# Optimization experiments

Measured on AMD Instinct MI355X. Metric: run time of the kernel, lower is better.

The kernel has to match this reference:

```python
import jax, jax.numpy as jnp
import numpy as np
import math

B, S, DIM = 2, 2048, 4096
N_HEADS, N_KV_HEADS = 32, 8
HEAD_DIM = DIM // N_HEADS  # 128
N_REP = N_HEADS // N_KV_HEADS  # 4
ROPE_THETA = 10000.0


def setup_inputs() -> dict:
    key = jax.random.key(0)
    ks = jax.random.split(key, 6)
    x = jax.random.normal(ks[0], (B, S, DIM), dtype=jnp.float32)
    wq = jax.random.normal(ks[1], (DIM, DIM), dtype=jnp.float32) * 0.02
    wk = jax.random.normal(ks[2], (N_KV_HEADS * HEAD_DIM, DIM), dtype=jnp.float32) * 0.02
    wv = jax.random.normal(ks[3], (N_KV_HEADS * HEAD_DIM, DIM), dtype=jnp.float32) * 0.02
    wo = jax.random.normal(ks[4], (DIM, DIM), dtype=jnp.float32) * 0.02
    # rotary freqs_cis (seqlen, head_dim//2), represented as cos/sin
    inv_freq = 1.0 / (ROPE_THETA ** (jnp.arange(0, HEAD_DIM, 2, dtype=jnp.float32) / HEAD_DIM))
    angles = jnp.arange(S, dtype=jnp.float32)[:, None] * inv_freq[None, :]  # [S, HEAD_DIM//2]
    freqs_cos = jnp.cos(angles)
    freqs_sin = jnp.sin(angles)
    # additive causal mask [S, S]: 0 on/below diagonal, -inf above
    mask = jnp.where(jnp.tril(jnp.ones((S, S), dtype=bool)), 0.0, -jnp.inf).astype(jnp.float32)
    return {"x": x, "wq": wq, "wk": wk, "wv": wv, "wo": wo,
            "freqs_cos": freqs_cos, "freqs_sin": freqs_sin, "mask": mask}


def _apply_rotary(t, freqs_cos, freqs_sin):
    # t: [B, S, H, HEAD_DIM]; interpret pairs (even, odd) as complex
    t2 = t.reshape(*t.shape[:-1], HEAD_DIM // 2, 2)
    tr, ti = t2[..., 0], t2[..., 1]
    c = freqs_cos[None, :, None, :]  # [1, S, 1, HD/2]
    s = freqs_sin[None, :, None, :]
    out_r = tr * c - ti * s
    out_i = tr * s + ti * c
    return jnp.stack([out_r, out_i], axis=-1).reshape(t.shape)


def reference(x, wq, wk, wv, wo, freqs_cos, freqs_sin, mask):
    bsz, seqlen, _ = x.shape
    xq = (x @ wq.T).reshape(bsz, seqlen, N_HEADS, HEAD_DIM)
    xk = (x @ wk.T).reshape(bsz, seqlen, N_KV_HEADS, HEAD_DIM)
    xv = (x @ wv.T).reshape(bsz, seqlen, N_KV_HEADS, HEAD_DIM)
    xq = _apply_rotary(xq, freqs_cos, freqs_sin)
    xk = _apply_rotary(xk, freqs_cos, freqs_sin)
    # repeat_kv (GQA): [B,S,KV,HD] -> [B,S,KV*N_REP,HD] via repeat_interleave on head axis
    keys = jnp.repeat(xk, N_REP, axis=2)
    values = jnp.repeat(xv, N_REP, axis=2)
    # scores: [B, H, S, S]
    scores = jnp.einsum('bqhd,bkhd->bhqk', xq, keys) / math.sqrt(HEAD_DIM)
    scores = scores + mask[None, None, :, :]
    probs = jax.nn.softmax(scores.astype(jnp.float32), axis=-1).astype(xq.dtype)
    out = jnp.einsum('bhqk,bkhd->bqhd', probs, values).reshape(bsz, seqlen, DIM)
    return out @ wo.T
```

## Files before the change

### kernel.cpp

```cpp
#include <hip/hip_runtime.h>

typedef __bf16 bf16;
typedef __bf16 bf16x4 __attribute__((ext_vector_type(4)));
typedef __bf16 bf16x8 __attribute__((ext_vector_type(8)));
typedef float f32x4 __attribute__((ext_vector_type(4)));

#define BB 2
#define SS 2048
#define DIM 4096
#define KVDIM 1024
#define NH 32
#define NKV 8
#define HD 128
#define NEGINF (-1e30f)

__device__ __forceinline__ void async16(void* lds, const void* gmem) {
    __builtin_amdgcn_global_load_lds(
        (const __attribute__((address_space(1))) void*)gmem,
        (__attribute__((address_space(3))) void*)lds, 16, 0, 0);
}

__device__ __forceinline__ f32x4 mfma16(bf16x8 a, bf16x8 b, f32x4 c) {
    return __builtin_amdgcn_mfma_f32_16x16x32_bf16(a, b, c, 0, 0, 0);
}

struct DetectArgs { const void* p[7]; int n[7]; };

__global__ void detect_dtypes(DetectArgs a, int* flags) {
    __shared__ int bad;
    const int ti = blockIdx.x;
    if (threadIdx.x == 0) bad = 0;
    __syncthreads();
    const bf16* s = (const bf16*)a.p[ti];
    int n = a.n[ti];
    int take = n < 8192 ? n : 8192;
    int lbad = 0;
    for (int i = threadIdx.x; i < take; i += 256) {
        float f = (float)s[i];
        if (!(f > -1e4f && f < 1e4f)) lbad = 1;
    }
    if (lbad) atomicOr(&bad, 1);
    __syncthreads();
    if (threadIdx.x == 0) flags[ti] = bad;
}

__global__ void convert_to_bf16(const void* __restrict__ src, bf16* __restrict__ dst,
                                int n8, const int* __restrict__ flagp) {
    int i = blockIdx.x * 256 + threadIdx.x;
    if (i >= n8) return;
    if (*flagp) {
        const float* s = (const float*)src + (size_t)i * 8;
        bf16x8 v;
#pragma unroll
        for (int j = 0; j < 8; ++j) v[j] = (bf16)s[j];
        *(bf16x8*)(dst + (size_t)i * 8) = v;
    } else {
        *(bf16x8*)(dst + (size_t)i * 8) = *((const bf16x8*)src + i);
    }
}

#define SBAR()  asm volatile("s_barrier" ::: "memory")
#define LGKM0() asm volatile("s_waitcnt lgkmcnt(0)" ::: "memory")
#define VM4()   asm volatile("s_waitcnt vmcnt(4)" ::: "memory")
#define VM0()   asm volatile("s_waitcnt vmcnt(0)" ::: "memory")

__device__ __forceinline__ void gemm256_core(const bf16* __restrict__ A,
                                             const bf16* __restrict__ B,
                                             int K, int m0, int n0,
                                             f32x4 (&acc)[8][4]) {
    __shared__ bf16 sm[2][4][8192];
    const int t = threadIdx.x;
    const int lane = t & 63;
    const int w = t >> 6;
    const int l15 = lane & 15, quad = lane >> 4;
    const int wm = w >> 2;
    const int wn = w & 3;
    const int axr = l15 & 7;
    const int c0 = (quad ^ axr) * 8;
    const int c1 = ((4 + quad) ^ axr) * 8;
    const int srl = t >> 3;
    const int sch = ((t & 7) ^ (srl & 7)) * 8;
    const size_t Ks = (size_t)K;

    bf16x8 aReg[4][2], bReg[4][2];

#define RD_A(c_, mh) { \
    const bf16* ab = &sm[c_][wm][0] + ((mh) * 64 + l15) * 64; \
    _Pragma("unroll") for (int i = 0; i < 4; ++i) { \
        aReg[i][0] = *(const bf16x8*)(ab + i * 1024 + c0); \
        aReg[i][1] = *(const bf16x8*)(ab + i * 1024 + c1); } }

#define RD_B(c_, nh) { \
    const bf16* bb = &sm[c_][2 + (wn >> 1)][0] + ((wn & 1) * 64 + (nh) * 32 + l15) * 64; \
    _Pragma("unroll") for (int jj = 0; jj < 2; ++jj) { \
        bReg[(nh) * 2 + jj][0] = *(const bf16x8*)(bb + jj * 1024 + c0); \
        bReg[(nh) * 2 + jj][1] = *(const bf16x8*)(bb + jj * 1024 + c1); } }

#define STG(c_, reg_, Mat, rowbase, kt) { \
    bf16* d_ = &sm[c_][reg_][0] + (size_t)t * 8; \
    const bf16* s_ = (Mat) + ((size_t)((rowbase) + srl)) * Ks + (size_t)(kt) * 64 + sch; \
    async16(d_, s_); \
    async16(d_ + 4096, s_ + 64 * Ks); }

#define MM(mh, nh) { \
    _Pragma("unroll") for (int i = 0; i < 4; ++i) \
    _Pragma("unroll") for (int jj = 0; jj < 2; ++jj) { \
        acc[(mh) * 4 + i][(nh) * 2 + jj] = \
            mfma16(aReg[i][0], bReg[(nh) * 2 + jj][0], acc[(mh) * 4 + i][(nh) * 2 + jj]); \
        acc[(mh) * 4 + i][(nh) * 2 + jj] = \
            mfma16(aReg[i][1], bReg[(nh) * 2 + jj][1], acc[(mh) * 4 + i][(nh) * 2 + jj]); } }

    STG(0, 0, A, m0, 0);
    STG(0, 2, B, n0, 0);
    STG(0, 1, A, m0 + 128, 0);
    STG(0, 3, B, n0 + 128, 0);
    STG(1, 2, B, n0, 1);
    STG(1, 0, A, m0, 1);
    VM4(); SBAR();

    const int NT = K >> 6;
    for (int T = 0; T < NT; ++T) {
        const int c = T & 1, nc = c ^ 1;
        const int kt1 = (T + 1 < NT) ? T + 1 : 0;
        const int kt2 = (T + 2 < NT) ? T + 2 : 0;
        RD_A(c, 0); RD_B(c, 0);
        STG(nc, 1, A, m0 + 128, kt1);
        SBAR();
        __builtin_amdgcn_s_setprio(1); MM(0, 0); __builtin_amdgcn_s_setprio(0);
        LGKM0(); SBAR();
        RD_B(c, 1);
        STG(nc, 3, B, n0 + 128, kt1);
        SBAR();
        __builtin_amdgcn_s_setprio(1); MM(0, 1); __builtin_amdgcn_s_setprio(0);
        LGKM0(); SBAR();
        RD_A(c, 1);
        STG(c, 2, B, n0, kt2);
        SBAR();
        __builtin_amdgcn_s_setprio(1); MM(1, 0); __builtin_amdgcn_s_setprio(0);
        LGKM0(); SBAR();
        STG(c, 0, A, m0, kt2);
        SBAR();
        __builtin_amdgcn_s_setprio(1); MM(1, 1); __builtin_amdgcn_s_setprio(0);
        LGKM0(); VM4(); SBAR();
    }
#undef RD_A
#undef RD_B
#undef STG
#undef MM
}

__global__ __launch_bounds__(512, 2)
void gemm_nt(const bf16* __restrict__ A, const bf16* __restrict__ B,
             bf16* __restrict__ C, int M, int N, int K) {
    const int t = threadIdx.x, lane = t & 63, w = t >> 6;
    const int l15 = lane & 15, quad = lane >> 4;
    const int wm = w >> 2, wn = w & 3;
    const int m0 = blockIdx.y * 256, n0 = blockIdx.x * 256;
    f32x4 acc[8][4] = {};
    gemm256_core(A, B, K, m0, n0, acc);
#pragma unroll
    for (int i = 0; i < 8; ++i)
#pragma unroll
        for (int j = 0; j < 4; ++j) {
            int col = n0 + wn * 64 + j * 16 + l15;
#pragma unroll
            for (int r = 0; r < 4; ++r)
                C[(size_t)(m0 + wm * 128 + i * 16 + quad * 4 + r) * N + col] = (bf16)acc[i][j][r];
        }
}

__global__ __launch_bounds__(512, 2)
void gemm_nt_kv(const bf16* __restrict__ A, const bf16* __restrict__ Bkv,
                bf16* __restrict__ Kc, bf16* __restrict__ Vc, int M, int K) {
    const int t = threadIdx.x, lane = t & 63, w = t >> 6;
    const int l15 = lane & 15, quad = lane >> 4;
    const int wm = w >> 2, wn = w & 3;
    const int m0 = blockIdx.y * 256, n0 = blockIdx.x * 256;
    f32x4 acc[8][4] = {};
    gemm256_core(A, Bkv, K, m0, n0, acc);
    bf16* C = (n0 < KVDIM) ? Kc : Vc;
    const int cb = (n0 < KVDIM) ? n0 : n0 - KVDIM;
#pragma unroll
    for (int i = 0; i < 8; ++i)
#pragma unroll
        for (int j = 0; j < 4; ++j) {
            int col = cb + wn * 64 + j * 16 + l15;
#pragma unroll
            for (int r = 0; r < 4; ++r)
                C[(size_t)(m0 + wm * 128 + i * 16 + quad * 4 + r) * KVDIM + col] = (bf16)acc[i][j][r];
        }
}

__global__ __launch_bounds__(512, 2)
void gemm_nt_out(const bf16* __restrict__ A, const bf16* __restrict__ B,
                 void* __restrict__ C, int M, int N, int K,
                 const int* __restrict__ flagp) {
    const int t = threadIdx.x, lane = t & 63, w = t >> 6;
    const int l15 = lane & 15, quad = lane >> 4;
    const int wm = w >> 2, wn = w & 3;
    const int m0 = blockIdx.y * 256, n0 = blockIdx.x * 256;
    const int f32out = *flagp;
    f32x4 acc[8][4] = {};
    gemm256_core(A, B, K, m0, n0, acc);
#pragma unroll
    for (int i = 0; i < 8; ++i)
#pragma unroll
        for (int j = 0; j < 4; ++j) {
            int col = n0 + wn * 64 + j * 16 + l15;
#pragma unroll
            for (int r = 0; r < 4; ++r) {
                int row = m0 + wm * 128 + i * 16 + quad * 4 + r;
                if (f32out) ((float*)C)[(size_t)row * N + col] = acc[i][j][r];
                else        ((bf16*)C)[(size_t)row * N + col] = (bf16)acc[i][j][r];
            }
        }
}

__device__ __forceinline__ void rope8(bf16* p, const bf16* fc, const bf16* fs,
                                      int s, int i0, float sc) {
    bf16x8 v = *(bf16x8*)p;
    bf16x8 o;
#pragma unroll
    for (int j = 0; j < 4; ++j) {
        float tr = (float)v[2 * j], ti = (float)v[2 * j + 1];
        float cc = (float)fc[s * 64 + i0 + j];
        float sn = (float)fs[s * 64 + i0 + j];
        o[2 * j]     = (bf16)((tr * cc - ti * sn) * sc);
        o[2 * j + 1] = (bf16)((tr * sn + ti * cc) * sc);
    }
    *(bf16x8*)p = o;
}

__global__ void rope_kernel(bf16* __restrict__ Q, bf16* __restrict__ Kr,
                            const bf16* __restrict__ fc, const bf16* __restrict__ fs) {
    const float qscale = 0.08838834764831845f * 1.4426950408889634f;
    int u = blockIdx.x * 256 + threadIdx.x;
    const int QU = (DIM * (BB * SS)) / 8;
    if (u < QU) {
        int row = u >> 9;
        int c = (u & 511) * 8;
        rope8(Q + (size_t)row * DIM + c, fc, fs, row & (SS - 1), (c >> 1) & 63, qscale);
    } else {
        u -= QU;
        int row = u >> 7;
        int c = (u & 127) * 8;
        rope8(Kr + (size_t)row * KVDIM + c, fc, fs, row & (SS - 1), (c >> 1) & 63, 1.0f);
    }
}

__global__ void transpose_v(const bf16* __restrict__ V, bf16* __restrict__ Vt) {
    __shared__ bf16 tile[64][74];
    const int st = blockIdx.x, ct = blockIdx.y, b = blockIdx.z;
    const int s0 = st * 64;
    const int kvh = ct >> 1, d0 = (ct & 1) * 64;
    const int t = threadIdx.x;
#pragma unroll
    for (int i = 0; i < 2; ++i) {
        int o = i * 256 + t;
        int r = o >> 3, c8 = (o & 7) * 8;
        bf16x8 v = *(const bf16x8*)(V + (size_t)(b * SS + s0 + r) * KVDIM + kvh * HD + d0 + c8);
#pragma unroll
        for (int j = 0; j < 8; ++j) tile[r][c8 + j] = v[j];
    }
    __syncthreads();
#pragma unroll
    for (int i = 0; i < 2; ++i) {
        int o = i * 256 + t;
        int sseg = (o & 7) * 8, dl = o >> 3;
        bf16x8 v;
#pragma unroll
        for (int j = 0; j < 8; ++j) v[j] = tile[sseg + j][dl];
        *(bf16x8*)(Vt + ((size_t)((b * NKV + kvh) * HD) + d0 + dl) * SS + s0 + sseg) = v;
    }
}

__global__ __launch_bounds__(256, 2)
void flash_attn(const bf16* __restrict__ Q, const bf16* __restrict__ Kr,
                const bf16* __restrict__ Vt, bf16* __restrict__ AO) {
    __shared__ char smem[32768];
    bf16* Ks  = (bf16*)smem;
    bf16* Vts = (bf16*)(smem + 16384);
    char* Ps  = smem;
    const int t = threadIdx.x, w = t >> 6, lane = t & 63;
    const int l15 = lane & 15, quad = lane >> 4;
    const int bh = blockIdx.x;
    const int b = bh >> 5, h = bh & 31, kvh = h >> 2;
    const int q0 = ((int)gridDim.y - 1 - (int)blockIdx.y) * 128;

    bf16x8 qf[2][4];
#pragma unroll
    for (int mi = 0; mi < 2; ++mi) {
        int qrow = b * SS + q0 + w * 32 + mi * 16 + l15;
#pragma unroll
        for (int ks = 0; ks < 4; ++ks)
            qf[mi][ks] = *(const bf16x8*)(Q + (size_t)qrow * DIM + h * HD + ks * 32 + quad * 8);
    }

    f32x4 of[2][8] = {};
    float mrow[2] = {NEGINF, NEGINF};
    float lrow[2] = {0.f, 0.f};

    const int kend = q0 + 128;
    for (int kk = 0; kk < kend; kk += 64) {
#pragma unroll
        for (int i = 0; i < 4; ++i) {
            int s = i * 256 + t;
            int key = s >> 4, slot = s & 15;
            int dseg = slot ^ (key & 15);
            async16((char*)Ks + (size_t)s * 16,
                    Kr + (size_t)(b * SS + kk + key) * KVDIM + kvh * HD + dseg * 8);
        }
#pragma unroll
        for (int i = 0; i < 4; ++i) {
            int s = i * 256 + t;
            int d = s >> 3, slot = s & 7;
            int kseg = slot ^ (d & 7);
            async16((char*)Vts + (size_t)s * 16,
                    Vt + ((size_t)((b * NKV + kvh) * HD + d)) * SS + kk + kseg * 8);
        }
        VM4(); SBAR();

        f32x4 sacc[2][4] = {};
#pragma unroll
        for (int nt = 0; nt < 4; ++nt) {
            int key = nt * 16 + l15;
#pragma unroll
            for (int ks = 0; ks < 4; ++ks) {
                int slot = (ks * 4 + quad) ^ (key & 15);
                bf16x8 kf = *(const bf16x8*)(Ks + key * 128 + slot * 8);
#pragma unroll
                for (int mi = 0; mi < 2; ++mi)
                    sacc[mi][nt] = mfma16(kf, qf[mi][ks], sacc[mi][nt]);
            }
        }
        if (kk >= q0) {
#pragma unroll
            for (int mi = 0; mi < 2; ++mi) {
                int q = q0 + w * 32 + mi * 16 + l15;
#pragma unroll
                for (int nt = 0; nt < 4; ++nt) {
                    int kbase = kk + nt * 16 + quad * 4;
#pragma unroll
                    for (int r = 0; r < 4; ++r)
                        if (kbase + r > q) sacc[mi][nt][r] = NEGINF;
                }
            }
        }
#pragma unroll
        for (int mi = 0; mi < 2; ++mi) {
            float m01[4];
#pragma unroll
            for (int nt = 0; nt < 4; ++nt)
                m01[nt] = fmaxf(fmaxf(sacc[mi][nt][0], sacc[mi][nt][1]),
                                fmaxf(sacc[mi][nt][2], sacc[mi][nt][3]));
            float mx = fmaxf(fmaxf(m01[0], m01[1]), fmaxf(m01[2], m01[3]));
            mx = fmaxf(mx, __shfl_xor(mx, 16));
            mx = fmaxf(mx, __shfl_xor(mx, 32));
            if (__all(mx - mrow[mi] <= 8.0f)) {
                float rs[4];
#pragma unroll
                for (int nt = 0; nt < 4; ++nt) {
                    rs[nt] = 0.f;
#pragma unroll
                    for (int r = 0; r < 4; ++r) {
                        float p = exp2f(sacc[mi][nt][r] - mrow[mi]);
                        sacc[mi][nt][r] = p;
                        rs[nt] += p;
                    }
                }
                float rsum = (rs[0] + rs[1]) + (rs[2] + rs[3]);
                rsum += __shfl_xor(rsum, 16);
                rsum += __shfl_xor(rsum, 32);
                lrow[mi] += rsum;
            } else {
                float mnew = fmaxf(mrow[mi], mx);
                float alpha = exp2f(mrow[mi] - mnew);
                float rs[4];
#pragma unroll
                for (int nt = 0; nt < 4; ++nt) {
                    rs[nt] = 0.f;
#pragma unroll
                    for (int r = 0; r < 4; ++r) {
                        float p = exp2f(sacc[mi][nt][r] - mnew);
                        sacc[mi][nt][r] = p;
                        rs[nt] += p;
                    }
                }
                float rsum = (rs[0] + rs[1]) + (rs[2] + rs[3]);
                rsum += __shfl_xor(rsum, 16);
                rsum += __shfl_xor(rsum, 32);
                lrow[mi] = lrow[mi] * alpha + rsum;
                mrow[mi] = mnew;
#pragma unroll
                for (int dt = 0; dt < 8; ++dt)
#pragma unroll
                    for (int r = 0; r < 4; ++r) of[mi][dt][r] *= alpha;
            }
        }
        VM0(); SBAR();
#pragma unroll
        for (int mi = 0; mi < 2; ++mi) {
            int row = w * 32 + mi * 16 + l15;
#pragma unroll
            for (int nt = 0; nt < 4; ++nt) {
                bf16x4 pv;
#pragma unroll
                for (int r = 0; r < 4; ++r) pv[r] = (bf16)sacc[mi][nt][r];
                int cc = nt * 2 + (quad >> 1);
                *(bf16x4*)(Ps + row * 128 + ((cc ^ (row & 7)) * 16 + (quad & 1) * 8)) = pv;
            }
        }
#pragma unroll
        for (int kb = 0; kb < 2; ++kb) {
            bf16x8 pa[2];
#pragma unroll
            for (int mi = 0; mi < 2; ++mi) {
                int row = w * 32 + mi * 16 + l15;
                pa[mi] = *(const bf16x8*)(Ps + row * 128 + (((kb * 4 + quad) ^ (row & 7)) * 16));
            }
#pragma unroll
            for (int dt = 0; dt < 8; ++dt) {
                int d = dt * 16 + l15;
                int slot = (kb * 4 + quad) ^ (d & 7);
                bf16x8 vb = *(const bf16x8*)(Vts + d * 64 + slot * 8);
#pragma unroll
                for (int mi = 0; mi < 2; ++mi)
                    of[mi][dt] = mfma16(vb, pa[mi], of[mi][dt]);
            }
        }
        SBAR();
    }
    bf16* Os = (bf16*)smem;
#pragma unroll
    for (int mi = 0; mi < 2; ++mi) {
        float inv = 1.0f / lrow[mi];
        int row = w * 32 + mi * 16 + l15;
#pragma unroll
        for (int dt = 0; dt < 8; ++dt) {
            bf16x4 o4;
#pragma unroll
            for (int r = 0; r < 4; ++r) o4[r] = (bf16)(of[mi][dt][r] * inv);
            int s = dt * 2 + (quad >> 1);
            int slot = s ^ l15;
            *(bf16x4*)((char*)Os + row * 256 + slot * 16 + (quad & 1) * 8) = o4;
        }
    }
    __syncthreads();
#pragma unroll
    for (int i = 0; i < 8; ++i) {
        int flat = i * 256 + t;
        int ql = flat >> 4, s = flat & 15;
        bf16x8 v = *(const bf16x8*)((char*)Os + ql * 256 + (s ^ (ql & 15)) * 16);
        *(bf16x8*)(AO + (size_t)(b * SS + q0 + ql) * DIM + h * HD + s * 8) = v;
    }
}

extern "C" void kernel_launch(void* const* d_in, const int* in_sizes, int n_in,
                              void* d_out, int out_size, void* d_ws, size_t ws_size,
                              hipStream_t stream) {
    const size_t MD = (size_t)BB * SS * DIM;
    const size_t KV = (size_t)BB * SS * KVDIM;
    const size_t FC = (size_t)SS * (HD / 2);
    const int M = BB * SS;

    int* flags = (int*)d_ws;
    bf16* xb  = (bf16*)((char*)d_ws + 32);
    bf16* wb  = xb + MD;
    bf16* Q   = wb + MD;
    bf16* Kr  = Q + MD;
    bf16* Vw  = Kr + KV;
    bf16* Vt  = Vw + KV;
    bf16* fcb = Vt + KV;
    bf16* fsb = fcb + FC;

    DetectArgs da;
    for (int i = 0; i < 7; ++i) { da.p[i] = d_in[i]; da.n[i] = in_sizes[i]; }
    detect_dtypes<<<7, 256, 0, stream>>>(da, flags);

    dim3 blk(256);
    dim3 blk512(512);
    convert_to_bf16<<<(int)(MD / 8 / 256), blk, 0, stream>>>(d_in[0], xb, (int)(MD / 8), flags + 0);
    convert_to_bf16<<<(int)(FC / 8 / 256), blk, 0, stream>>>(d_in[5], fcb, (int)(FC / 8), flags + 5);
    convert_to_bf16<<<(int)(FC / 8 / 256), blk, 0, stream>>>(d_in[6], fsb, (int)(FC / 8), flags + 6);

    convert_to_bf16<<<(int)(MD / 8 / 256), blk, 0, stream>>>(d_in[1], wb, (int)(MD / 8), flags + 1);
    gemm_nt<<<dim3(DIM / 256, M / 256), blk512, 0, stream>>>(xb, wb, Q, M, DIM, DIM);

    convert_to_bf16<<<(int)(KV / 8 / 256), blk, 0, stream>>>(d_in[2], wb, (int)(KV / 8), flags + 2);
    convert_to_bf16<<<(int)(KV / 8 / 256), blk, 0, stream>>>(d_in[3], wb + KV, (int)(KV / 8), flags + 3);
    gemm_nt_kv<<<dim3(2 * KVDIM / 256, M / 256), blk512, 0, stream>>>(xb, wb, Kr, Vw, M, DIM);

    rope_kernel<<<dim3((int)((MD / 8 + KV / 8) / 256)), blk, 0, stream>>>(Q, Kr, fcb, fsb);
    transpose_v<<<dim3(SS / 64, 16, BB), blk, 0, stream>>>(Vw, Vt);

    flash_attn<<<dim3(BB * NH, SS / 128), blk, 0, stream>>>(Q, Kr, Vt, xb);

    convert_to_bf16<<<(int)(MD / 8 / 256), blk, 0, stream>>>(d_in[4], wb, (int)(MD / 8), flags + 4);
    gemm_nt_out<<<dim3(DIM / 256, M / 256), blk512, 0, stream>>>(xb, wb, d_out, M, DIM, DIM, flags + 0);
}
```

Before: 734.3 us.

## Double-buffer K tiles in flash attention and merge small launch kernels

```diff
diff --git a/kernel.cpp b/kernel.cpp
--- a/kernel.cpp
+++ b/kernel.cpp
@@ -44,23 +44,42 @@
     if (threadIdx.x == 0) flags[ti] = bad;
 }
 
+__device__ __forceinline__ void conv8(const void* src, bf16* dst, int rel, int flag) {
+    if (flag) {
+        const float* s = (const float*)src + (size_t)rel * 8;
+        bf16x8 v;
+#pragma unroll
+        for (int j = 0; j < 8; ++j) v[j] = (bf16)s[j];
+        *(bf16x8*)(dst + (size_t)rel * 8) = v;
+    } else {
+        *(bf16x8*)(dst + (size_t)rel * 8) = *((const bf16x8*)src + rel);
+    }
+}
+
 __global__ void convert_to_bf16(const void* __restrict__ src, bf16* __restrict__ dst,
                                 int n8, const int* __restrict__ flagp) {
     int i = blockIdx.x * 256 + threadIdx.x;
     if (i >= n8) return;
-    if (*flagp) {
-        const float* s = (const float*)src + (size_t)i * 8;
-        bf16x8 v;
-#pragma unroll
-        for (int j = 0; j < 8; ++j) v[j] = (bf16)s[j];
-        *(bf16x8*)(dst + (size_t)i * 8) = v;
-    } else {
-        *(bf16x8*)(dst + (size_t)i * 8) = *((const bf16x8*)src + i);
-    }
+    conv8(src, dst, i, *flagp);
+}
+
+__global__ void convert4(const void* s0, bf16* d0, int n0, const int* f0,
+                         const void* s1, bf16* d1, int n1, const int* f1,
+                         const void* s2, bf16* d2, int n2, const int* f2,
+                         const void* s3, bf16* d3, int n3, const int* f3) {
+    int u = blockIdx.x * 256 + threadIdx.x;
+    if (u < n0)                       { conv8(s0, d0, u, *f0); return; }
+    u -= n0;
+    if (u < n1)                       { conv8(s1, d1, u, *f1); return; }
+    u -= n1;
+    if (u < n2)                       { conv8(s2, d2, u, *f2); return; }
+    u -= n2;
+    if (u < n3)                       { conv8(s3, d3, u, *f3); return; }
 }
 
 #define SBAR()  asm volatile("s_barrier" ::: "memory")
 #define LGKM0() asm volatile("s_waitcnt lgkmcnt(0)" ::: "memory")
+#define VM8()   asm volatile("s_waitcnt vmcnt(8)" ::: "memory")
 #define VM4()   asm volatile("s_waitcnt vmcnt(4)" ::: "memory")
 #define VM0()   asm volatile("s_waitcnt vmcnt(0)" ::: "memory")
 
@@ -231,29 +250,34 @@
     *(bf16x8*)p = o;
 }
 
-__global__ void rope_kernel(bf16* __restrict__ Q, bf16* __restrict__ Kr,
-                            const bf16* __restrict__ fc, const bf16* __restrict__ fs) {
-    const float qscale = 0.08838834764831845f * 1.4426950408889634f;
-    int u = blockIdx.x * 256 + threadIdx.x;
-    const int QU = (DIM * (BB * SS)) / 8;
-    if (u < QU) {
-        int row = u >> 9;
-        int c = (u & 511) * 8;
-        rope8(Q + (size_t)row * DIM + c, fc, fs, row & (SS - 1), (c >> 1) & 63, qscale);
-    } else {
-        u -= QU;
-        int row = u >> 7;
-        int c = (u & 127) * 8;
-        rope8(Kr + (size_t)row * KVDIM + c, fc, fs, row & (SS - 1), (c >> 1) & 63, 1.0f);
-    }
-}
-
-__global__ void transpose_v(const bf16* __restrict__ V, bf16* __restrict__ Vt) {
+#define ROPE_BLOCKS ((DIM * (BB * SS) / 8 + KVDIM * (BB * SS) / 8) / 256)
+
+__global__ void rope_tv(bf16* __restrict__ Q, bf16* __restrict__ Kr,
+                        const bf16* __restrict__ fc, const bf16* __restrict__ fs,
+                        const bf16* __restrict__ V, bf16* __restrict__ Vt) {
     __shared__ bf16 tile[64][74];
-    const int st = blockIdx.x, ct = blockIdx.y, b = blockIdx.z;
+    const int bid = blockIdx.x;
+    const int t = threadIdx.x;
+    if (bid < ROPE_BLOCKS) {
+        const float qscale = 0.08838834764831845f * 1.4426950408889634f;
+        int u = bid * 256 + t;
+        const int QU = (DIM * (BB * SS)) / 8;
+        if (u < QU) {
+            int row = u >> 9;
+            int c = (u & 511) * 8;
+            rope8(Q + (size_t)row * DIM + c, fc, fs, row & (SS - 1), (c >> 1) & 63, qscale);
+        } else {
+            u -= QU;
+            int row = u >> 7;
+            int c = (u & 127) * 8;
+            rope8(Kr + (size_t)row * KVDIM + c, fc, fs, row & (SS - 1), (c >> 1) & 63, 1.0f);
+        }
+        return;
+    }
+    const int b2 = bid - ROPE_BLOCKS;
+    const int st = b2 & 31, ct = (b2 >> 5) & 15, b = b2 >> 9;
     const int s0 = st * 64;
     const int kvh = ct >> 1, d0 = (ct & 1) * 64;
-    const int t = threadIdx.x;
 #pragma unroll
     for (int i = 0; i < 2; ++i) {
         int o = i * 256 + t;
@@ -277,16 +301,30 @@
 __global__ __launch_bounds__(256, 2)
 void flash_attn(const bf16* __restrict__ Q, const bf16* __restrict__ Kr,
                 const bf16* __restrict__ Vt, bf16* __restrict__ AO) {
-    __shared__ char smem[32768];
-    bf16* Ks  = (bf16*)smem;
-    bf16* Vts = (bf16*)(smem + 16384);
-    char* Ps  = smem;
+    __shared__ char smem[49152];
+    bf16* Vts = (bf16*)(smem + 32768);
     const int t = threadIdx.x, w = t >> 6, lane = t & 63;
     const int l15 = lane & 15, quad = lane >> 4;
     const int bh = blockIdx.x;
     const int b = bh >> 5, h = bh & 31, kvh = h >> 2;
     const int q0 = ((int)gridDim.y - 1 - (int)blockIdx.y) * 128;
 
+#define STAGE_K(kb_, kk_) { \
+    char* kbase_ = smem + (kb_) * 16384; \
+    _Pragma("unroll") for (int i = 0; i < 4; ++i) { \
+        int s_ = i * 256 + t; \
+        int key_ = s_ >> 4, slot_ = s_ & 15; \
+        int dseg_ = slot_ ^ (key_ & 15); \
+        async16(kbase_ + (size_t)s_ * 16, \
+                Kr + (size_t)(b * SS + (kk_) + key_) * KVDIM + kvh * HD + dseg_ * 8); } }
+#define STAGE_V(kk_) { \
+    _Pragma("unroll") for (int i = 0; i < 4; ++i) { \
+        int s_ = i * 256 + t; \
+        int d_ = s_ >> 3, slot_ = s_ & 7; \
+        int kseg_ = slot_ ^ (d_ & 7); \
+        async16((char*)Vts + (size_t)s_ * 16, \
+                Vt + ((size_t)((b * NKV + kvh) * HD + d_)) * SS + (kk_) + kseg_ * 8); } }
+
     bf16x8 qf[2][4];
 #pragma unroll
     for (int mi = 0; mi < 2; ++mi) {
@@ -300,37 +338,28 @@
     float mrow[2] = {NEGINF, NEGINF};
     float lrow[2] = {0.f, 0.f};
 
-    const int kend = q0 + 128;
-    for (int kk = 0; kk < kend; kk += 64) {
-#pragma unroll
-        for (int i = 0; i < 4; ++i) {
-            int s = i * 256 + t;
-            int key = s >> 4, slot = s & 15;
-            int dseg = slot ^ (key & 15);
-            async16((char*)Ks + (size_t)s * 16,
-                    Kr + (size_t)(b * SS + kk + key) * KVDIM + kvh * HD + dseg * 8);
-        }
-#pragma unroll
-        for (int i = 0; i < 4; ++i) {
-            int s = i * 256 + t;
-            int d = s >> 3, slot = s & 7;
-            int kseg = slot ^ (d & 7);
-            async16((char*)Vts + (size_t)s * 16,
-                    Vt + ((size_t)((b * NKV + kvh) * HD + d)) * SS + kk + kseg * 8);
-        }
-        VM4(); SBAR();
+    const int nt = (q0 + 128) >> 6;
+    STAGE_K(0, 0);
+    for (int ti = 0; ti < nt; ++ti) {
+        const int kk = ti << 6;
+        const int cur = ti & 1, nxt = cur ^ 1;
+        bf16* Ks = (bf16*)(smem + cur * 16384);
+        char* Ps = smem + cur * 16384;
+        STAGE_V(kk);
+        STAGE_K(nxt, (ti + 1 < nt) ? kk + 64 : 0);
+        VM8(); SBAR();
 
         f32x4 sacc[2][4] = {};
 #pragma unroll
-        for (int nt = 0; nt < 4; ++nt) {
-            int key = nt * 16 + l15;
+        for (int nt2 = 0; nt2 < 4; ++nt2) {
+            int key = nt2 * 16 + l15;
 #pragma unroll
             for (int ks = 0; ks < 4; ++ks) {
                 int slot = (ks * 4 + quad) ^ (key & 15);
                 bf16x8 kf = *(const bf16x8*)(Ks + key * 128 + slot * 8);
 #pragma unroll
                 for (int mi = 0; mi < 2; ++mi)
-                    sacc[mi][nt] = mfma16(kf, qf[mi][ks], sacc[mi][nt]);
+                    sacc[mi][nt2] = mfma16(kf, qf[mi][ks], sacc[mi][nt2]);
             }
         }
         if (kk >= q0) {
@@ -338,11 +367,11 @@
             for (int mi = 0; mi < 2; ++mi) {
                 int q = q0 + w * 32 + mi * 16 + l15;
 #pragma unroll
-                for (int nt = 0; nt < 4; ++nt) {
-                    int kbase = kk + nt * 16 + quad * 4;
+                for (int nt2 = 0; nt2 < 4; ++nt2) {
+                    int kbase = kk + nt2 * 16 + quad * 4;
 #pragma unroll
                     for (int r = 0; r < 4; ++r)
-                        if (kbase + r > q) sacc[mi][nt][r] = NEGINF;
+                        if (kbase + r > q) sacc[mi][nt2][r] = NEGINF;
                 }
             }
         }
@@ -350,22 +379,22 @@
         for (int mi = 0; mi < 2; ++mi) {
             float m01[4];
 #pragma unroll
-            for (int nt = 0; nt < 4; ++nt)
-                m01[nt] = fmaxf(fmaxf(sacc[mi][nt][0], sacc[mi][nt][1]),
-                                fmaxf(sacc[mi][nt][2], sacc[mi][nt][3]));
+            for (int nt2 = 0; nt2 < 4; ++nt2)
+                m01[nt2] = fmaxf(fmaxf(sacc[mi][nt2][0], sacc[mi][nt2][1]),
+                                 fmaxf(sacc[mi][nt2][2], sacc[mi][nt2][3]));
             float mx = fmaxf(fmaxf(m01[0], m01[1]), fmaxf(m01[2], m01[3]));
             mx = fmaxf(mx, __shfl_xor(mx, 16));
             mx = fmaxf(mx, __shfl_xor(mx, 32));
             if (__all(mx - mrow[mi] <= 8.0f)) {
                 float rs[4];
 #pragma unroll
-                for (int nt = 0; nt < 4; ++nt) {
-                    rs[nt] = 0.f;
+                for (int nt2 = 0; nt2 < 4; ++nt2) {
+                    rs[nt2] = 0.f;
 #pragma unroll
                     for (int r = 0; r < 4; ++r) {
-                        float p = exp2f(sacc[mi][nt][r] - mrow[mi]);
-                        sacc[mi][nt][r] = p;
-                        rs[nt] += p;
+                        float p = exp2f(sacc[mi][nt2][r] - mrow[mi]);
+                        sacc[mi][nt2][r] = p;
+                        rs[nt2] += p;
                     }
                 }
                 float rsum = (rs[0] + rs[1]) + (rs[2] + rs[3]);
@@ -377,13 +406,13 @@
                 float alpha = exp2f(mrow[mi] - mnew);
                 float rs[4];
 #pragma unroll
-                for (int nt = 0; nt < 4; ++nt) {
-                    rs[nt] = 0.f;
+                for (int nt2 = 0; nt2 < 4; ++nt2) {
+                    rs[nt2] = 0.f;
 #pragma unroll
                     for (int r = 0; r < 4; ++r) {
-                        float p = exp2f(sacc[mi][nt][r] - mnew);
-                        sacc[mi][nt][r] = p;
-                        rs[nt] += p;
+                        float p = exp2f(sacc[mi][nt2][r] - mnew);
+                        sacc[mi][nt2][r] = p;
+                        rs[nt2] += p;
                     }
                 }
                 float rsum = (rs[0] + rs[1]) + (rs[2] + rs[3]);
@@ -397,16 +426,16 @@
                     for (int r = 0; r < 4; ++r) of[mi][dt][r] *= alpha;
             }
         }
-        VM0(); SBAR();
+        VM4(); SBAR();
 #pragma unroll
         for (int mi = 0; mi < 2; ++mi) {
             int row = w * 32 + mi * 16 + l15;
 #pragma unroll
-            for (int nt = 0; nt < 4; ++nt) {
+            for (int nt2 = 0; nt2 < 4; ++nt2) {
                 bf16x4 pv;
 #pragma unroll
-                for (int r = 0; r < 4; ++r) pv[r] = (bf16)sacc[mi][nt][r];
-                int cc = nt * 2 + (quad >> 1);
+                for (int r = 0; r < 4; ++r) pv[r] = (bf16)sacc[mi][nt2][r];
+                int cc = nt2 * 2 + (quad >> 1);
                 *(bf16x4*)(Ps + row * 128 + ((cc ^ (row & 7)) * 16 + (quad & 1) * 8)) = pv;
             }
         }
@@ -430,6 +459,9 @@
         }
         SBAR();
     }
+    VM0(); SBAR();
+#undef STAGE_K
+#undef STAGE_V
     bf16* Os = (bf16*)smem;
 #pragma unroll
     for (int mi = 0; mi < 2; ++mi) {
@@ -479,19 +511,28 @@
 
     dim3 blk(256);
     dim3 blk512(512);
-    convert_to_bf16<<<(int)(MD / 8 / 256), blk, 0, stream>>>(d_in[0], xb, (int)(MD / 8), flags + 0);
-    convert_to_bf16<<<(int)(FC / 8 / 256), blk, 0, stream>>>(d_in[5], fcb, (int)(FC / 8), flags + 5);
-    convert_to_bf16<<<(int)(FC / 8 / 256), blk, 0, stream>>>(d_in[6], fsb, (int)(FC / 8), flags + 6);
-
-    convert_to_bf16<<<(int)(MD / 8 / 256), blk, 0, stream>>>(d_in[1], wb, (int)(MD / 8), flags + 1);
+
+    {
+        int n0 = (int)(MD / 8), n1 = (int)(FC / 8), n2 = (int)(FC / 8), n3 = (int)(MD / 8);
+        int nb = (n0 + n1 + n2 + n3 + 255) / 256;
+        convert4<<<nb, blk, 0, stream>>>(d_in[0], xb, n0, flags + 0,
+                                         d_in[5], fcb, n1, flags + 5,
+                                         d_in[6], fsb, n2, flags + 6,
+                                         d_in[1], wb, n3, flags + 1);
+    }
     gemm_nt<<<dim3(DIM / 256, M / 256), blk512, 0, stream>>>(xb, wb, Q, M, DIM, DIM);
 
-    convert_to_bf16<<<(int)(KV / 8 / 256), blk, 0, stream>>>(d_in[2], wb, (int)(KV / 8), flags + 2);
-    convert_to_bf16<<<(int)(KV / 8 / 256), blk, 0, stream>>>(d_in[3], wb + KV, (int)(KV / 8), flags + 3);
+    {
+        int n0 = (int)(KV / 8), n1 = (int)(KV / 8);
+        int nb = (n0 + n1 + 255) / 256;
+        convert4<<<nb, blk, 0, stream>>>(d_in[2], wb, n0, flags + 2,
+                                         d_in[3], wb + KV, n1, flags + 3,
+                                         nullptr, nullptr, 0, flags + 2,
+                                         nullptr, nullptr, 0, flags + 2);
+    }
     gemm_nt_kv<<<dim3(2 * KVDIM / 256, M / 256), blk512, 0, stream>>>(xb, wb, Kr, Vw, M, DIM);
 
-    rope_kernel<<<dim3((int)((MD / 8 + KV / 8) / 256)), blk, 0, stream>>>(Q, Kr, fcb, fsb);
-    transpose_v<<<dim3(SS / 64, 16, BB), blk, 0, stream>>>(Vw, Vt);
+    rope_tv<<<dim3(ROPE_BLOCKS + (SS / 64) * 16 * BB), blk, 0, stream>>>(Q, Kr, fcb, fsb, Vw, Vt);
 
     flash_attn<<<dim3(BB * NH, SS / 128), blk, 0, stream>>>(Q, Kr, Vt, xb);
 
```

After: 727.7 us. About the same (-0.9%).

## Fuse QKV projections into one GEMM and merge conversion and rope/transpose launches

Applied to the files above, without the earlier changes.

```diff
diff --git a/kernel.cpp b/kernel.cpp
--- a/kernel.cpp
+++ b/kernel.cpp
@@ -9,6 +9,7 @@
 #define SS 2048
 #define DIM 4096
 #define KVDIM 1024
+#define QKVN (DIM + 2 * KVDIM)
 #define NH 32
 #define NKV 8
 #define HD 128
@@ -44,18 +45,33 @@
     if (threadIdx.x == 0) flags[ti] = bad;
 }
 
+__device__ __forceinline__ void conv8(const void* src, bf16* dst, int rel, int flag) {
+    if (flag) {
+        const float* s = (const float*)src + (size_t)rel * 8;
+        bf16x8 v;
+#pragma unroll
+        for (int j = 0; j < 8; ++j) v[j] = (bf16)s[j];
+        *(bf16x8*)(dst + (size_t)rel * 8) = v;
+    } else {
+        *(bf16x8*)(dst + (size_t)rel * 8) = *((const bf16x8*)src + rel);
+    }
+}
+
 __global__ void convert_to_bf16(const void* __restrict__ src, bf16* __restrict__ dst,
                                 int n8, const int* __restrict__ flagp) {
     int i = blockIdx.x * 256 + threadIdx.x;
     if (i >= n8) return;
-    if (*flagp) {
-        const float* s = (const float*)src + (size_t)i * 8;
-        bf16x8 v;
-#pragma unroll
-        for (int j = 0; j < 8; ++j) v[j] = (bf16)s[j];
-        *(bf16x8*)(dst + (size_t)i * 8) = v;
-    } else {
-        *(bf16x8*)(dst + (size_t)i * 8) = *((const bf16x8*)src + i);
+    conv8(src, dst, i, *flagp);
+}
+
+struct Conv6 { const void* s[6]; bf16* d[6]; int n[6]; const int* f[6]; };
+
+__global__ void convert6(Conv6 c) {
+    int u = blockIdx.x * 256 + threadIdx.x;
+#pragma unroll
+    for (int i = 0; i < 6; ++i) {
+        if (u < c.n[i]) { conv8(c.s[i], c.d[i], u, *c.f[i]); return; }
+        u -= c.n[i];
     }
 }
 
@@ -150,36 +166,21 @@
 }
 
 __global__ __launch_bounds__(512, 2)
-void gemm_nt(const bf16* __restrict__ A, const bf16* __restrict__ B,
-             bf16* __restrict__ C, int M, int N, int K) {
+void gemm_qkv(const bf16* __restrict__ A, const bf16* __restrict__ Bqkv,
+              bf16* __restrict__ Qo, bf16* __restrict__ Kc, bf16* __restrict__ Vc,
+              int M, int K) {
     const int t = threadIdx.x, lane = t & 63, w = t >> 6;
     const int l15 = lane & 15, quad = lane >> 4;
     const int wm = w >> 2, wn = w & 3;
     const int m0 = blockIdx.y * 256, n0 = blockIdx.x * 256;
     f32x4 acc[8][4] = {};
-    gemm256_core(A, B, K, m0, n0, acc);
-#pragma unroll
-    for (int i = 0; i < 8; ++i)
-#pragma unroll
-        for (int j = 0; j < 4; ++j) {
-            int col = n0 + wn * 64 + j * 16 + l15;
-#pragma unroll
-            for (int r = 0; r < 4; ++r)
-                C[(size_t)(m0 + wm * 128 + i * 16 + quad * 4 + r) * N + col] = (bf16)acc[i][j][r];
-        }
-}
-
-__global__ __launch_bounds__(512, 2)
-void gemm_nt_kv(const bf16* __restrict__ A, const bf16* __restrict__ Bkv,
-                bf16* __restrict__ Kc, bf16* __restrict__ Vc, int M, int K) {
-    const int t = threadIdx.x, lane = t & 63, w = t >> 6;
-    const int l15 = lane & 15, quad = lane >> 4;
-    const int wm = w >> 2, wn = w & 3;
-    const int m0 = blockIdx.y * 256, n0 = blockIdx.x * 256;
-    f32x4 acc[8][4] = {};
-    gemm256_core(A, Bkv, K, m0, n0, acc);
-    bf16* C = (n0 < KVDIM) ? Kc : Vc;
-    const int cb = (n0 < KVDIM) ? n0 : n0 - KVDIM;
+    gemm256_core(A, Bqkv, K, m0, n0, acc);
+    bf16* C;
+    int cb;
+    size_t ldc;
+    if (n0 < DIM)               { C = Qo; cb = n0;                ldc = DIM; }
+    else if (n0 < DIM + KVDIM)  { C = Kc; cb = n0 - DIM;          ldc = KVDIM; }
+    else                        { C = Vc; cb = n0 - DIM - KVDIM;  ldc = KVDIM; }
 #pragma unroll
     for (int i = 0; i < 8; ++i)
 #pragma unroll
@@ -187,7 +188,7 @@
             int col = cb + wn * 64 + j * 16 + l15;
 #pragma unroll
             for (int r = 0; r < 4; ++r)
-                C[(size_t)(m0 + wm * 128 + i * 16 + quad * 4 + r) * KVDIM + col] = (bf16)acc[i][j][r];
+                C[(size_t)(m0 + wm * 128 + i * 16 + quad * 4 + r) * ldc + col] = (bf16)acc[i][j][r];
         }
 }
 
@@ -231,29 +232,34 @@
     *(bf16x8*)p = o;
 }
 
-__global__ void rope_kernel(bf16* __restrict__ Q, bf16* __restrict__ Kr,
-                            const bf16* __restrict__ fc, const bf16* __restrict__ fs) {
-    const float qscale = 0.08838834764831845f * 1.4426950408889634f;
-    int u = blockIdx.x * 256 + threadIdx.x;
-    const int QU = (DIM * (BB * SS)) / 8;
-    if (u < QU) {
-        int row = u >> 9;
-        int c = (u & 511) * 8;
-        rope8(Q + (size_t)row * DIM + c, fc, fs, row & (SS - 1), (c >> 1) & 63, qscale);
-    } else {
-        u -= QU;
-        int row = u >> 7;
-        int c = (u & 127) * 8;
-        rope8(Kr + (size_t)row * KVDIM + c, fc, fs, row & (SS - 1), (c >> 1) & 63, 1.0f);
-    }
-}
-
-__global__ void transpose_v(const bf16* __restrict__ V, bf16* __restrict__ Vt) {
+#define ROPE_BLOCKS ((DIM * (BB * SS) / 8 + KVDIM * (BB * SS) / 8) / 256)
+
+__global__ void rope_tv(bf16* __restrict__ Q, bf16* __restrict__ Kr,
+                        const bf16* __restrict__ fc, const bf16* __restrict__ fs,
+                        const bf16* __restrict__ V, bf16* __restrict__ Vt) {
     __shared__ bf16 tile[64][74];
-    const int st = blockIdx.x, ct = blockIdx.y, b = blockIdx.z;
+    const int bid = blockIdx.x;
+    const int t = threadIdx.x;
+    if (bid < ROPE_BLOCKS) {
+        const float qscale = 0.08838834764831845f * 1.4426950408889634f;
+        int u = bid * 256 + t;
+        const int QU = (DIM * (BB * SS)) / 8;
+        if (u < QU) {
+            int row = u >> 9;
+            int c = (u & 511) * 8;
+            rope8(Q + (size_t)row * DIM + c, fc, fs, row & (SS - 1), (c >> 1) & 63, qscale);
+        } else {
+            u -= QU;
+            int row = u >> 7;
+            int c = (u & 127) * 8;
+            rope8(Kr + (size_t)row * KVDIM + c, fc, fs, row & (SS - 1), (c >> 1) & 63, 1.0f);
+        }
+        return;
+    }
+    const int b2 = bid - ROPE_BLOCKS;
+    const int st = b2 & 31, ct = (b2 >> 5) & 15, b = b2 >> 9;
     const int s0 = st * 64;
     const int kvh = ct >> 1, d0 = (ct & 1) * 64;
-    const int t = threadIdx.x;
 #pragma unroll
     for (int i = 0; i < 2; ++i) {
         int o = i * 256 + t;
@@ -460,13 +466,14 @@
                               hipStream_t stream) {
     const size_t MD = (size_t)BB * SS * DIM;
     const size_t KV = (size_t)BB * SS * KVDIM;
+    const size_t WQKV = (size_t)QKVN * DIM;
     const size_t FC = (size_t)SS * (HD / 2);
     const int M = BB * SS;
 
     int* flags = (int*)d_ws;
     bf16* xb  = (bf16*)((char*)d_ws + 32);
     bf16* wb  = xb + MD;
-    bf16* Q   = wb + MD;
+    bf16* Q   = wb + WQKV;
     bf16* Kr  = Q + MD;
     bf16* Vw  = Kr + KV;
     bf16* Vt  = Vw + KV;
@@ -479,19 +486,22 @@
 
     dim3 blk(256);
     dim3 blk512(512);
-    convert_to_bf16<<<(int)(MD / 8 / 256), blk, 0, stream>>>(d_in[0], xb, (int)(MD / 8), flags + 0);
-    convert_to_bf16<<<(int)(FC / 8 / 256), blk, 0, stream>>>(d_in[5], fcb, (int)(FC / 8), flags + 5);
-    convert_to_bf16<<<(int)(FC / 8 / 256), blk, 0, stream>>>(d_in[6], fsb, (int)(FC / 8), flags + 6);
-
-    convert_to_bf16<<<(int)(MD / 8 / 256), blk, 0, stream>>>(d_in[1], wb, (int)(MD / 8), flags + 1);
-    gemm_nt<<<dim3(DIM / 256, M / 256), blk512, 0, stream>>>(xb, wb, Q, M, DIM, DIM);
-
-    convert_to_bf16<<<(int)(KV / 8 / 256), blk, 0, stream>>>(d_in[2], wb, (int)(KV / 8), flags + 2);
-    convert_to_bf16<<<(int)(KV / 8 / 256), blk, 0, stream>>>(d_in[3], wb + KV, (int)(KV / 8), flags + 3);
-    gemm_nt_kv<<<dim3(2 * KVDIM / 256, M / 256), blk512, 0, stream>>>(xb, wb, Kr, Vw, M, DIM);
-
-    rope_kernel<<<dim3((int)((MD / 8 + KV / 8) / 256)), blk, 0, stream>>>(Q, Kr, fcb, fsb);
-    transpose_v<<<dim3(SS / 64, 16, BB), blk, 0, stream>>>(Vw, Vt);
+
+    {
+        Conv6 c;
+        c.s[0] = d_in[0]; c.d[0] = xb;            c.n[0] = (int)(MD / 8); c.f[0] = flags + 0;
+        c.s[1] = d_in[1]; c.d[1] = wb;            c.n[1] = (int)(MD / 8); c.f[1] = flags + 1;
+        c.s[2] = d_in[2]; c.d[2] = wb + MD;       c.n[2] = (int)(KV / 8); c.f[2] = flags + 2;
+        c.s[3] = d_in[3]; c.d[3] = wb + MD + KV;  c.n[3] = (int)(KV / 8); c.f[3] = flags + 3;
+        c.s[4] = d_in[5]; c.d[4] = fcb;           c.n[4] = (int)(FC / 8); c.f[4] = flags + 5;
+        c.s[5] = d_in[6]; c.d[5] = fsb;           c.n[5] = (int)(FC / 8); c.f[5] = flags + 6;
+        long total = 2L * (MD / 8) + 2L * (KV / 8) + 2L * (FC / 8);
+        convert6<<<(int)((total + 255) / 256), blk, 0, stream>>>(c);
+    }
+
+    gemm_qkv<<<dim3(QKVN / 256, M / 256), blk512, 0, stream>>>(xb, wb, Q, Kr, Vw, M, DIM);
+
+    rope_tv<<<dim3(ROPE_BLOCKS + (SS / 64) * 16 * BB), blk, 0, stream>>>(Q, Kr, fcb, fsb, Vw, Vt);
 
     flash_attn<<<dim3(BB * NH, SS / 128), blk, 0, stream>>>(Q, Kr, Vt, xb);
 
```

After: 711.4 us. 3.1% less time.
